# Performance work log

Measured on AMD Instinct MI355X. Metric: run time of the kernel, lower is better.

Reference implementation:

```python
import jax, jax.numpy as jnp
import numpy as np

B, S, D, N, LAYERS = 512, 64, 256, 100000, 1


def setup_inputs() -> dict:
    key = jax.random.key(0)
    ks = jax.random.split(key, 9)
    stdv = 1.0 / np.sqrt(D)
    return {
        "embedding": jax.random.uniform(ks[0], (N, D), jnp.float32, -stdv, stdv),
        "W1": jax.random.uniform(ks[1], (2 * D, 2 * D), jnp.float32, -stdv, stdv),
        "W2": jax.random.uniform(ks[2], (2 * D, D), jnp.float32, -stdv, stdv),
        "adj_in": jax.random.uniform(ks[3], (B, S, S), jnp.float32),
        "adj_out": jax.random.uniform(ks[4], (B, S, S), jnp.float32),
        "mask": jnp.ones((B, S), jnp.float32),
        "item": jax.random.randint(ks[5], (B, S), 0, N),
        "alias": jax.random.randint(ks[6], (B, S), 0, S),
        "tar": jax.random.randint(ks[7], (B,), 1, N),  # targets in [1, n_node)
    }


def reference(embedding, W1, W2, adj_in, adj_out, mask, item, alias, tar):
    # ---- sgc(): gather -> dual adjacency aggregation -> concat -> 2-layer MLP
    fin = embedding[item]                              # [B,S,D]
    # torch `adj ** layers` is elementwise power (not matrix power)
    fs_in = jnp.matmul(adj_in ** LAYERS, fin)          # [B,S,D]
    fs_out = jnp.matmul(adj_out ** LAYERS, fin)        # [B,S,D]
    av = jnp.concatenate([fs_in, fs_out], axis=-1)     # [B,S,2D]
    av = jnp.matmul(jax.nn.relu(jnp.matmul(av, W1)), W2)  # [B,S,D]

    # ---- forward(): pick last node's hidden, score against item table
    rows = jnp.arange(B)
    rm = jnp.sum(mask, axis=1).astype(jnp.int32)       # session lengths [B]
    last_id = alias[rows, rm - 1]                      # [B]
    last_h = av[rows, last_id]                         # [B,D]
    logits = last_h @ embedding[1:].T                  # [B,N-1]

    logp = jax.nn.log_softmax(logits, axis=-1)
    loss = -jnp.mean(logp[rows, tar - 1])
    # L2 term is zero: params live in a plain dict (not registered) and l2=0.
    return loss, logits
```

## Files before the change

### kernel.cpp

```cpp
#include <hip/hip_runtime.h>
#include <hip/hip_bf16.h>
#include <cstdint>
#include <cstddef>

#define BDIM 512
#define SDIM 64
#define DDIM 256
#define D2   512
#define NNODE 100000
#define NM1  99999

typedef short short8 __attribute__((ext_vector_type(8)));
typedef float f32x4 __attribute__((ext_vector_type(4)));

__device__ __forceinline__ unsigned short f2bf(float f) {
  unsigned int u = __float_as_uint(f);
  u += 0x7FFFu + ((u >> 16) & 1u);
  return (unsigned short)(u >> 16);
}

__global__ __launch_bounds__(256) void prep_kernel(
    const float* __restrict__ emb, const float* __restrict__ adj_in,
    const float* __restrict__ adj_out, const float* __restrict__ mask,
    const int* __restrict__ item, const int* __restrict__ alias_,
    float* __restrict__ av) {
  __shared__ float a_in[SDIM], a_out[SDIM];
  __shared__ int it[SDIM];
  __shared__ int s_star;
  const int b = blockIdx.x, t = threadIdx.x;
  if (t < SDIM) it[t] = item[b * SDIM + t];
  if (t == 0) {
    float s = 0.f;
    for (int j = 0; j < SDIM; j++) s += mask[b * SDIM + j];
    int rm = (int)s;
    s_star = alias_[b * SDIM + rm - 1];
  }
  __syncthreads();
  const int ss = s_star;
  if (t < SDIM) a_in[t] = adj_in[((size_t)b * SDIM + ss) * SDIM + t];
  else if (t < 2 * SDIM) a_out[t - SDIM] = adj_out[((size_t)b * SDIM + ss) * SDIM + (t - SDIM)];
  __syncthreads();
  const int d = t;
  float ai = 0.f, ao = 0.f;
#pragma unroll 8
  for (int j = 0; j < SDIM; j++) {
    float e = emb[(size_t)it[j] * DDIM + d];
    ai = fmaf(a_in[j], e, ai);
    ao = fmaf(a_out[j], e, ao);
  }
  av[(size_t)b * D2 + d] = ai;
  av[(size_t)b * D2 + DDIM + d] = ao;
}

__global__ __launch_bounds__(256) void mlp1_kernel(
    const float* __restrict__ A, const float* __restrict__ W,
    float* __restrict__ O) {
  __shared__ float As[16][16];
  __shared__ float Bs[16][17];
  const int tx = threadIdx.x, ty = threadIdx.y;
  const int row = blockIdx.y * 16 + ty, col = blockIdx.x * 16 + tx;
  float acc = 0.f;
  for (int k0 = 0; k0 < D2; k0 += 16) {
    As[ty][tx] = A[(size_t)row * D2 + k0 + tx];
    Bs[ty][tx] = W[(size_t)(k0 + ty) * D2 + col];
    __syncthreads();
#pragma unroll
    for (int k = 0; k < 16; k++) acc = fmaf(As[ty][k], Bs[k][tx], acc);
    __syncthreads();
  }
  O[(size_t)row * D2 + col] = fmaxf(acc, 0.f);
}

__global__ __launch_bounds__(256) void mlp2_kernel(
    const float* __restrict__ A, const float* __restrict__ W,
    unsigned short* __restrict__ O) {
  __shared__ float As[16][16];
  __shared__ float Bs[16][17];
  const int tx = threadIdx.x, ty = threadIdx.y;
  const int row = blockIdx.y * 16 + ty, col = blockIdx.x * 16 + tx;
  float acc = 0.f;
  for (int k0 = 0; k0 < D2; k0 += 16) {
    As[ty][tx] = A[(size_t)row * D2 + k0 + tx];
    Bs[ty][tx] = W[(size_t)(k0 + ty) * DDIM + col];
    __syncthreads();
#pragma unroll
    for (int k = 0; k < 16; k++) acc = fmaf(As[ty][k], Bs[k][tx], acc);
    __syncthreads();
  }
  O[(size_t)row * DDIM + col] = f2bf(acc);
}

#define LDA 72
__global__ __launch_bounds__(256) void logits_gemm(
    const unsigned short* __restrict__ Abf,
    const float* __restrict__ emb,
    float* __restrict__ out,
    float* __restrict__ rse) {
  __shared__ short As[128 * LDA];
  __shared__ short Bs[128 * LDA];
  const int t = threadIdx.x;
  const int mbase = blockIdx.x * 128;
  const int nbase = blockIdx.y * 128;
  const int lane = t & 63, w = t >> 6;
  const int wm = (w >> 1) * 64, wn = (w & 1) * 64;
  const int c = lane & 15, q = lane >> 4;

  f32x4 acc[4][4];
#pragma unroll
  for (int mi = 0; mi < 4; mi++)
#pragma unroll
    for (int ni = 0; ni < 4; ni++) acc[mi][ni] = (f32x4){0.f, 0.f, 0.f, 0.f};

  const int r8 = t >> 3;
  const int kcol = (t & 7) * 8;

  for (int k0 = 0; k0 < DDIM; k0 += 64) {
    __syncthreads();
#pragma unroll
    for (int i = 0; i < 4; i++) {
      const int row = i * 32 + r8;
      const short8 a8 = *(const short8*)(Abf + (size_t)(mbase + row) * DDIM + k0 + kcol);
      *(short8*)&As[row * LDA + kcol] = a8;
      const int n = nbase + row;
      const int er = (n + 1 <= NM1) ? (n + 1) : NM1;
      const float* bg = emb + (size_t)er * DDIM + k0 + kcol;
      const float4 b0 = *(const float4*)bg;
      const float4 b1 = *(const float4*)(bg + 4);
      short8 p;
      p[0] = (short)f2bf(b0.x); p[1] = (short)f2bf(b0.y);
      p[2] = (short)f2bf(b0.z); p[3] = (short)f2bf(b0.w);
      p[4] = (short)f2bf(b1.x); p[5] = (short)f2bf(b1.y);
      p[6] = (short)f2bf(b1.z); p[7] = (short)f2bf(b1.w);
      *(short8*)&Bs[row * LDA + kcol] = p;
    }
    __syncthreads();
#pragma unroll
    for (int kk = 0; kk < 64; kk += 32) {
      short8 afr[4], bfr[4];
#pragma unroll
      for (int mi = 0; mi < 4; mi++)
        afr[mi] = *(const short8*)&As[(wm + mi * 16 + c) * LDA + kk + q * 8];
#pragma unroll
      for (int ni = 0; ni < 4; ni++)
        bfr[ni] = *(const short8*)&Bs[(wn + ni * 16 + c) * LDA + kk + q * 8];
#pragma unroll
      for (int mi = 0; mi < 4; mi++)
#pragma unroll
        for (int ni = 0; ni < 4; ni++)
          acc[mi][ni] = __builtin_amdgcn_mfma_f32_16x16x32_bf16(
              afr[mi], bfr[ni], acc[mi][ni], 0, 0, 0);
    }
  }

#pragma unroll
  for (int mi = 0; mi < 4; mi++) {
#pragma unroll
    for (int r = 0; r < 4; r++) {
      const int grow = mbase + wm + mi * 16 + q * 4 + r;
      float s = 0.f;
#pragma unroll
      for (int ni = 0; ni < 4; ni++) {
        const int col = nbase + wn + ni * 16 + c;
        if (col < NM1) {
          const float v = acc[mi][ni][r];
          out[1 + (size_t)grow * NM1 + col] = v;
          s += __expf(v);
        }
      }
#pragma unroll
      for (int msk = 1; msk < 16; msk <<= 1) s += __shfl_xor(s, msk, 64);
      if (c == 0) atomicAdd(&rse[grow], s);
    }
  }
}

__global__ __launch_bounds__(512) void loss_kernel(
    float* __restrict__ out, const float* __restrict__ rse,
    const int* __restrict__ tar) {
  __shared__ float red[512];
  const int t = threadIdx.x;
  const int tt = tar[t];
  const float lg = out[1 + (size_t)t * NM1 + (tt - 1)];
  red[t] = logf(rse[t]) - lg;
  __syncthreads();
  for (int stride = 256; stride > 0; stride >>= 1) {
    if (t < stride) red[t] += red[t + stride];
    __syncthreads();
  }
  if (t == 0) out[0] = red[0] / (float)BDIM;
}

extern "C" void kernel_launch(void* const* d_in, const int* in_sizes, int n_in,
                              void* d_out, int out_size, void* d_ws, size_t ws_size,
                              hipStream_t stream) {
  const float* emb     = (const float*)d_in[0];
  const float* W1      = (const float*)d_in[1];
  const float* W2      = (const float*)d_in[2];
  const float* adj_in  = (const float*)d_in[3];
  const float* adj_out = (const float*)d_in[4];
  const float* mask    = (const float*)d_in[5];
  const int*   item    = (const int*)d_in[6];
  const int*   alias_  = (const int*)d_in[7];
  const int*   tar     = (const int*)d_in[8];
  float* out = (float*)d_out;

  char* ws = (char*)d_ws;
  float* av            = (float*)(ws);
  float* h1            = (float*)(ws + 1048576);
  unsigned short* lasth = (unsigned short*)(ws + 2097152);
  float* rse           = (float*)(ws + 2359296);

  hipMemsetAsync(rse, 0, BDIM * sizeof(float), stream);
  prep_kernel<<<BDIM, 256, 0, stream>>>(emb, adj_in, adj_out, mask, item, alias_, av);
  mlp1_kernel<<<dim3(32, 32), dim3(16, 16), 0, stream>>>(av, W1, h1);
  mlp2_kernel<<<dim3(16, 32), dim3(16, 16), 0, stream>>>(h1, W2, lasth);
  logits_gemm<<<dim3(4, 782), 256, 0, stream>>>(lasth, emb, out, rse);
  loss_kernel<<<1, 512, 0, stream>>>(out, rse, tar);
}
```

Measured before the change: 506.5 us.

## Restructure logits GEMM to convert each embedding tile once; register-tile MLP kernels

The logits GEMM now gives each block a 64-column embedding tile, converted to bf16 into LDS once, and loops over all 512 rows. A-fragments are read straight from global memory and outputs use nontemporal stores. Before, each embedding tile was re-read and re-converted by four M-blocks. The MLP kernels are merged into one templated kernel with 2x4 register tiling and float4 loads, and the mask sum uses a wavefront shuffle reduction. The cost is A-operand loads from global/L2 in the inner loop and fewer, larger MLP blocks.

```diff
diff --git a/kernel.cpp b/kernel.cpp
--- a/kernel.cpp
+++ b/kernel.cpp
@@ -1,5 +1,4 @@
 #include <hip/hip_runtime.h>
-#include <hip/hip_bf16.h>
 #include <cstdint>
 #include <cstddef>
 
@@ -29,11 +28,14 @@
   __shared__ int s_star;
   const int b = blockIdx.x, t = threadIdx.x;
   if (t < SDIM) it[t] = item[b * SDIM + t];
-  if (t == 0) {
-    float s = 0.f;
-    for (int j = 0; j < SDIM; j++) s += mask[b * SDIM + j];
-    int rm = (int)s;
-    s_star = alias_[b * SDIM + rm - 1];
+  if (t < 64) {
+    float m = mask[b * SDIM + t];
+#pragma unroll
+    for (int off = 32; off > 0; off >>= 1) m += __shfl_down(m, off, 64);
+    if (t == 0) {
+      int rm = (int)m;
+      s_star = alias_[b * SDIM + rm - 1];
+    }
   }
   __syncthreads();
   const int ss = s_star;
@@ -52,124 +54,140 @@
   av[(size_t)b * D2 + DDIM + d] = ao;
 }
 
-__global__ __launch_bounds__(256) void mlp1_kernel(
+template <int N, bool RELU, bool OUTBF16>
+__global__ __launch_bounds__(256) void mlp_kernel(
     const float* __restrict__ A, const float* __restrict__ W,
-    float* __restrict__ O) {
-  __shared__ float As[16][16];
-  __shared__ float Bs[16][17];
+    float* __restrict__ Of, unsigned short* __restrict__ Ob) {
+  __shared__ float As[32][36];
+  __shared__ float Bs[32][68];
   const int tx = threadIdx.x, ty = threadIdx.y;
-  const int row = blockIdx.y * 16 + ty, col = blockIdx.x * 16 + tx;
-  float acc = 0.f;
-  for (int k0 = 0; k0 < D2; k0 += 16) {
-    As[ty][tx] = A[(size_t)row * D2 + k0 + tx];
-    Bs[ty][tx] = W[(size_t)(k0 + ty) * D2 + col];
+  const int t = ty * 16 + tx;
+  const int row0 = blockIdx.y * 32, col0 = blockIdx.x * 64;
+  const int ar = t >> 3, ac = (t & 7) * 4;
+  const int kr = t >> 4, bc = (t & 15) * 4;
+  float acc[2][4];
+#pragma unroll
+  for (int i = 0; i < 2; i++)
+#pragma unroll
+    for (int j = 0; j < 4; j++) acc[i][j] = 0.f;
+
+  for (int k0 = 0; k0 < D2; k0 += 32) {
+    const float4 a4 = *(const float4*)&A[(size_t)(row0 + ar) * D2 + k0 + ac];
+    const float4 b4a = *(const float4*)&W[(size_t)(k0 + kr) * N + col0 + bc];
+    const float4 b4b = *(const float4*)&W[(size_t)(k0 + kr + 16) * N + col0 + bc];
+    *(float4*)&As[ar][ac] = a4;
+    *(float4*)&Bs[kr][bc] = b4a;
+    *(float4*)&Bs[kr + 16][bc] = b4b;
     __syncthreads();
 #pragma unroll
-    for (int k = 0; k < 16; k++) acc = fmaf(As[ty][k], Bs[k][tx], acc);
+    for (int k = 0; k < 32; k++) {
+      const float a0 = As[ty * 2][k];
+      const float a1 = As[ty * 2 + 1][k];
+      const float4 bv = *(const float4*)&Bs[k][tx * 4];
+      acc[0][0] = fmaf(a0, bv.x, acc[0][0]); acc[0][1] = fmaf(a0, bv.y, acc[0][1]);
+      acc[0][2] = fmaf(a0, bv.z, acc[0][2]); acc[0][3] = fmaf(a0, bv.w, acc[0][3]);
+      acc[1][0] = fmaf(a1, bv.x, acc[1][0]); acc[1][1] = fmaf(a1, bv.y, acc[1][1]);
+      acc[1][2] = fmaf(a1, bv.z, acc[1][2]); acc[1][3] = fmaf(a1, bv.w, acc[1][3]);
+    }
     __syncthreads();
   }
-  O[(size_t)row * D2 + col] = fmaxf(acc, 0.f);
-}
-
-__global__ __launch_bounds__(256) void mlp2_kernel(
-    const float* __restrict__ A, const float* __restrict__ W,
-    unsigned short* __restrict__ O) {
-  __shared__ float As[16][16];
-  __shared__ float Bs[16][17];
-  const int tx = threadIdx.x, ty = threadIdx.y;
-  const int row = blockIdx.y * 16 + ty, col = blockIdx.x * 16 + tx;
-  float acc = 0.f;
-  for (int k0 = 0; k0 < D2; k0 += 16) {
-    As[ty][tx] = A[(size_t)row * D2 + k0 + tx];
-    Bs[ty][tx] = W[(size_t)(k0 + ty) * DDIM + col];
-    __syncthreads();
-#pragma unroll
-    for (int k = 0; k < 16; k++) acc = fmaf(As[ty][k], Bs[k][tx], acc);
-    __syncthreads();
-  }
-  O[(size_t)row * DDIM + col] = f2bf(acc);
-}
-
-#define LDA 72
-__global__ __launch_bounds__(256) void logits_gemm(
+#pragma unroll
+  for (int i = 0; i < 2; i++) {
+    const int row = row0 + ty * 2 + i;
+    const int col = col0 + tx * 4;
+    float4 r4;
+    r4.x = acc[i][0]; r4.y = acc[i][1]; r4.z = acc[i][2]; r4.w = acc[i][3];
+    if constexpr (RELU) {
+      r4.x = fmaxf(r4.x, 0.f); r4.y = fmaxf(r4.y, 0.f);
+      r4.z = fmaxf(r4.z, 0.f); r4.w = fmaxf(r4.w, 0.f);
+    }
+    if constexpr (OUTBF16) {
+      ushort4 p;
+      p.x = f2bf(r4.x); p.y = f2bf(r4.y); p.z = f2bf(r4.z); p.w = f2bf(r4.w);
+      *(ushort4*)&Ob[(size_t)row * N + col] = p;
+    } else {
+      *(float4*)&Of[(size_t)row * N + col] = r4;
+    }
+  }
+}
+
+#define NT    64
+#define BPAD  264
+#define NTILES 1563
+
+__global__ __launch_bounds__(256, 4) void logits_gemm(
     const unsigned short* __restrict__ Abf,
     const float* __restrict__ emb,
     float* __restrict__ out,
     float* __restrict__ rse) {
-  __shared__ short As[128 * LDA];
-  __shared__ short Bs[128 * LDA];
+  __shared__ short Bs[NT * BPAD];
   const int t = threadIdx.x;
-  const int mbase = blockIdx.x * 128;
-  const int nbase = blockIdx.y * 128;
   const int lane = t & 63, w = t >> 6;
-  const int wm = (w >> 1) * 64, wn = (w & 1) * 64;
+  const int nbase = blockIdx.x * NT;
+
+  {
+    const int r0 = w * 16;
+#pragma unroll 4
+    for (int i = 0; i < 16; i++) {
+      const int row = r0 + i;
+      int er = nbase + row + 1;
+      if (er > NM1) er = NM1;
+      const float4 v = *(const float4*)(emb + (size_t)er * DDIM + lane * 4);
+      ushort4 p;
+      p.x = f2bf(v.x); p.y = f2bf(v.y); p.z = f2bf(v.z); p.w = f2bf(v.w);
+      *(ushort4*)&Bs[row * BPAD + lane * 4] = p;
+    }
+  }
+  __syncthreads();
+
+  const int wm = (w >> 1) * 64;
+  const int wn = (w & 1) * 32;
   const int c = lane & 15, q = lane >> 4;
 
-  f32x4 acc[4][4];
-#pragma unroll
-  for (int mi = 0; mi < 4; mi++)
-#pragma unroll
-    for (int ni = 0; ni < 4; ni++) acc[mi][ni] = (f32x4){0.f, 0.f, 0.f, 0.f};
-
-  const int r8 = t >> 3;
-  const int kcol = (t & 7) * 8;
-
-  for (int k0 = 0; k0 < DDIM; k0 += 64) {
-    __syncthreads();
-#pragma unroll
-    for (int i = 0; i < 4; i++) {
-      const int row = i * 32 + r8;
-      const short8 a8 = *(const short8*)(Abf + (size_t)(mbase + row) * DDIM + k0 + kcol);
-      *(short8*)&As[row * LDA + kcol] = a8;
-      const int n = nbase + row;
-      const int er = (n + 1 <= NM1) ? (n + 1) : NM1;
-      const float* bg = emb + (size_t)er * DDIM + k0 + kcol;
-      const float4 b0 = *(const float4*)bg;
-      const float4 b1 = *(const float4*)(bg + 4);
-      short8 p;
-      p[0] = (short)f2bf(b0.x); p[1] = (short)f2bf(b0.y);
-      p[2] = (short)f2bf(b0.z); p[3] = (short)f2bf(b0.w);
-      p[4] = (short)f2bf(b1.x); p[5] = (short)f2bf(b1.y);
-      p[6] = (short)f2bf(b1.z); p[7] = (short)f2bf(b1.w);
-      *(short8*)&Bs[row * LDA + kcol] = p;
-    }
-    __syncthreads();
-#pragma unroll
-    for (int kk = 0; kk < 64; kk += 32) {
-      short8 afr[4], bfr[4];
+  for (int m = 0; m < 4; m++) {
+    f32x4 acc[4][2];
+#pragma unroll
+    for (int mi = 0; mi < 4; mi++)
+#pragma unroll
+      for (int ni = 0; ni < 2; ni++) acc[mi][ni] = (f32x4){0.f, 0.f, 0.f, 0.f};
+
+#pragma unroll
+    for (int ks = 0; ks < 8; ks++) {
+      short8 afr[4], bfr[2];
 #pragma unroll
       for (int mi = 0; mi < 4; mi++)
-        afr[mi] = *(const short8*)&As[(wm + mi * 16 + c) * LDA + kk + q * 8];
-#pragma unroll
-      for (int ni = 0; ni < 4; ni++)
-        bfr[ni] = *(const short8*)&Bs[(wn + ni * 16 + c) * LDA + kk + q * 8];
+        afr[mi] = *(const short8*)(Abf +
+            (size_t)(m * 128 + wm + mi * 16 + c) * DDIM + ks * 32 + q * 8);
+#pragma unroll
+      for (int ni = 0; ni < 2; ni++)
+        bfr[ni] = *(const short8*)&Bs[(wn + ni * 16 + c) * BPAD + ks * 32 + q * 8];
 #pragma unroll
       for (int mi = 0; mi < 4; mi++)
 #pragma unroll
-        for (int ni = 0; ni < 4; ni++)
+        for (int ni = 0; ni < 2; ni++)
           acc[mi][ni] = __builtin_amdgcn_mfma_f32_16x16x32_bf16(
               afr[mi], bfr[ni], acc[mi][ni], 0, 0, 0);
     }
-  }
-
-#pragma unroll
-  for (int mi = 0; mi < 4; mi++) {
-#pragma unroll
-    for (int r = 0; r < 4; r++) {
-      const int grow = mbase + wm + mi * 16 + q * 4 + r;
-      float s = 0.f;
-#pragma unroll
-      for (int ni = 0; ni < 4; ni++) {
-        const int col = nbase + wn + ni * 16 + c;
-        if (col < NM1) {
-          const float v = acc[mi][ni][r];
-          out[1 + (size_t)grow * NM1 + col] = v;
-          s += __expf(v);
+
+#pragma unroll
+    for (int mi = 0; mi < 4; mi++) {
+#pragma unroll
+      for (int r = 0; r < 4; r++) {
+        const int grow = m * 128 + wm + mi * 16 + q * 4 + r;
+        float s = 0.f;
+#pragma unroll
+        for (int ni = 0; ni < 2; ni++) {
+          const int col = nbase + wn + ni * 16 + c;
+          if (col < NM1) {
+            const float v = acc[mi][ni][r];
+            __builtin_nontemporal_store(v, &out[1 + (size_t)grow * NM1 + col]);
+            s += __expf(v);
+          }
         }
+#pragma unroll
+        for (int msk = 1; msk < 16; msk <<= 1) s += __shfl_xor(s, msk, 64);
+        if (c == 0) atomicAdd(&rse[grow], s);
       }
-#pragma unroll
-      for (int msk = 1; msk < 16; msk <<= 1) s += __shfl_xor(s, msk, 64);
-      if (c == 0) atomicAdd(&rse[grow], s);
     }
   }
 }
@@ -212,8 +230,8 @@
 
   hipMemsetAsync(rse, 0, BDIM * sizeof(float), stream);
   prep_kernel<<<BDIM, 256, 0, stream>>>(emb, adj_in, adj_out, mask, item, alias_, av);
-  mlp1_kernel<<<dim3(32, 32), dim3(16, 16), 0, stream>>>(av, W1, h1);
-  mlp2_kernel<<<dim3(16, 32), dim3(16, 16), 0, stream>>>(h1, W2, lasth);
-  logits_gemm<<<dim3(4, 782), 256, 0, stream>>>(lasth, emb, out, rse);
+  mlp_kernel<D2, true, false><<<dim3(8, 16), dim3(16, 16), 0, stream>>>(av, W1, h1, nullptr);
+  mlp_kernel<DDIM, false, true><<<dim3(4, 16), dim3(16, 16), 0, stream>>>(h1, W2, nullptr, lasth);
+  logits_gemm<<<dim3(NTILES), 256, 0, stream>>>(lasth, emb, out, rse);
   loss_kernel<<<1, 512, 0, stream>>>(out, rse, tar);
 }
```

After: 910.8 us. 79.8% more time.
